# Kernel tuning notes

Measured on AMD Instinct MI355X. Metric: run time of the kernel, lower is better.

Reference implementation:

```python
import jax, jax.numpy as jnp
import numpy as np

B, H, W, C = 2, 192, 192, 192
WS, SHIFT, NH = 16, 8, 6


def _window_partition(x, ws):
    b, h, w, c = x.shape
    x = x.reshape(b, h // ws, ws, w // ws, ws, c)
    return x.transpose(0, 1, 3, 2, 4, 5).reshape(-1, ws, ws, c)


def _window_reverse(win, ws, h, w):
    b = win.shape[0] // ((h // ws) * (w // ws))
    x = win.reshape(b, h // ws, w // ws, ws, ws, -1)
    return x.transpose(0, 1, 3, 2, 4, 5).reshape(b, h, w, -1)


def _relative_position_index(ws):
    coords = np.stack(np.meshgrid(np.arange(ws), np.arange(ws), indexing="ij"))
    cf = coords.reshape(2, -1)
    rel = (cf[:, :, None] - cf[:, None, :]).transpose(1, 2, 0).astype(np.int64)
    rel[..., 0] += ws - 1
    rel[..., 1] += ws - 1
    rel[..., 0] *= 2 * ws - 1
    return rel.sum(-1)  # (ws*ws, ws*ws) in [0, (2ws-1)^2)


def _shift_attn_mask(h, w, ws, shift):
    img = np.zeros((1, h, w, 1), np.float32)
    cnt = 0
    for hs in (slice(0, -ws), slice(-ws, -shift), slice(-shift, None)):
        for wsl in (slice(0, -ws), slice(-ws, -shift), slice(-shift, None)):
            img[:, hs, wsl, :] = cnt
            cnt += 1
    mw = np.asarray(_window_partition(jnp.asarray(img), ws)).reshape(-1, ws * ws)
    diff = mw[:, None, :] - mw[:, :, None]
    return jnp.asarray(np.where(diff != 0, -100.0, 0.0).astype(np.float32))


def setup_inputs():
    key = jax.random.key(0)
    ks = jax.random.split(key, 4)
    x = jax.random.normal(ks[0], (B, H, W, C), jnp.float32)
    qkv = jax.random.normal(ks[1], (B, H, W, 3 * C), jnp.float32)
    rpb_table = 0.02 * jax.random.normal(ks[2], ((2 * WS - 1) ** 2, NH), jnp.float32)
    geo_scale = jnp.full((NH,), 0.01, jnp.float32)
    geo_sigma = jnp.asarray(1.0, jnp.float32)
    proj_w = 0.02 * jax.random.normal(ks[3], (C, C), jnp.float32)
    proj_b = jnp.zeros((C,), jnp.float32)
    rpi = jnp.asarray(_relative_position_index(WS), jnp.int32)
    attn_mask = _shift_attn_mask(H, W, WS, SHIFT)
    return dict(x=x, qkv=qkv, rpb_table=rpb_table, geo_scale=geo_scale,
                geo_sigma=geo_sigma, proj_w=proj_w, proj_b=proj_b,
                rpi=rpi, attn_mask=attn_mask,
                window_size=WS, shift_size=SHIFT, num_heads=NH)


def _geo_bias(f, ws, sigma):
    # f: (nwb, ws, ws, C). L-shaped geodesic path: horizontal then vertical cumsums.
    nwb = f.shape[0]
    diff_h = jnp.sum(jnp.abs(f[:, :, 1:] - f[:, :, :-1]), -1)  # (nwb, ws, ws-1)
    ct_h = jnp.cumsum(jnp.concatenate(
        [jnp.zeros((nwb, ws, 1), f.dtype), 1.0 + sigma * diff_h], -1), -1)
    diff_v = jnp.sum(jnp.abs(f[:, 1:] - f[:, :-1]), -1)        # (nwb, ws-1, ws)
    ct_v = jnp.cumsum(jnp.concatenate(
        [jnp.zeros((nwb, 1, ws), f.dtype), 1.0 + sigma * diff_v], -2), -2)
    idx = jnp.arange(ws * ws)
    rows, cols = idx // ws, idx % ws
    ct_h_flat = ct_h[:, rows, cols]                    # (nwb, n)
    ct_v_flat = ct_v[:, rows, cols]
    ct_h_corner = ct_h[:, rows[:, None], cols[None, :]]  # ct_h[ri, cj] -> (nwb, n, n)
    ct_v_corner = ct_v[:, rows[:, None], cols[None, :]]
    geo_h = jnp.abs(ct_h_corner - ct_h_flat[:, :, None])
    geo_v = jnp.abs(ct_v_flat[:, None, :] - ct_v_corner)
    return geo_h + geo_v                               # (nwb, n, n)


def _forward(x, qkv, rpb_table, geo_scale, geo_sigma, proj_w, proj_b,
             rpi, attn_mask, ws, shift, nh):
    b, h, w, c = x.shape
    n = ws * ws
    hd = c // nh
    sx = jnp.roll(x, (-shift, -shift), (1, 2))
    sqkv = jnp.roll(qkv, (-shift, -shift), (1, 2))
    f_win = _window_partition(sx, ws)                           # (nwb, ws, ws, c)
    geo = _geo_bias(f_win, ws, jnp.abs(geo_sigma))              # (nwb, n, n)
    qkv_win = _window_partition(sqkv, ws).reshape(-1, n, 3, nh, hd)
    q = qkv_win[:, :, 0].transpose(0, 2, 1, 3)                  # (nwb, nh, n, hd)
    k = qkv_win[:, :, 1].transpose(0, 2, 1, 3)
    v = qkv_win[:, :, 2].transpose(0, 2, 1, 3)
    attn = jnp.einsum("bhqd,bhkd->bhqk", q * (hd ** -0.5), k)   # (nwb, nh, n, n)
    rpb = rpb_table[rpi.reshape(-1)].reshape(n, n, nh).transpose(2, 0, 1)
    attn = attn + rpb[None]
    attn = attn - geo[:, None] * geo_scale[None, :, None, None]
    nw = attn_mask.shape[0]
    attn = attn.reshape(b, nw, nh, n, n) + attn_mask[None, :, None]
    attn = jax.nn.softmax(attn.reshape(-1, nh, n, n), axis=-1)
    out = jnp.einsum("bhqk,bhkd->bqhd", attn, v).reshape(-1, n, c)
    out = out @ proj_w.T + proj_b                               # nn.Linear
    out = _window_reverse(out.reshape(-1, ws, ws, c), ws, h, w)
    out = jnp.roll(out, (shift, shift), (1, 2))
    return out.reshape(b, h * w, c)


def reference(x, qkv, rpb_table, geo_scale, geo_sigma, proj_w, proj_b,
              rpi, attn_mask, window_size, shift_size, num_heads):
    return _forward(x, qkv, rpb_table, geo_scale, geo_sigma, proj_w, proj_b,
                    rpi, attn_mask, window_size, shift_size, num_heads)
```

## Files before the change

### kernel.cpp

```cpp
#include <hip/hip_runtime.h>
#include <stdint.h>

#define HH 192
#define WWW 192
#define CC 192
#define WS 16
#define SHIFTS 8
#define NH 6
#define HD 32
#define NN 256
#define NWS 12
#define NWIN_B 144
#define NWIN 288
#define CTN (NWIN * NN)

typedef _Float16 half_t;
typedef half_t half2_t __attribute__((ext_vector_type(2)));
typedef half_t f16x8 __attribute__((ext_vector_type(8)));
typedef float f32x4 __attribute__((ext_vector_type(4)));
typedef uint32_t u32x4 __attribute__((ext_vector_type(4)));

#define LOG2E 1.4426950408889634f

#if __has_builtin(__builtin_amdgcn_exp2f)
#define EXP2F(x) __builtin_amdgcn_exp2f(x)
#else
#define EXP2F(x) __expf(0.6931471805599453f * (x))
#endif

__device__ __forceinline__ float sat16(float a) {
    return fminf(fmaxf(a, -60000.f), 60000.f);
}
__device__ __forceinline__ uint32_t pack_h2(float a, float b) {
    half2_t h; h.x = (half_t)sat16(a); h.y = (half_t)sat16(b);
    return __builtin_bit_cast(uint32_t, h);
}
__device__ __forceinline__ uint32_t pack_p(float a, float b) {
    half2_t h; h.x = (half_t)a; h.y = (half_t)b;
    return __builtin_bit_cast(uint32_t, h);
}

__device__ __forceinline__ size_t xrow(int b, int sh, int sw) {
    int oh = sh + SHIFTS; if (oh >= HH) oh -= HH;
    int ow = sw + SHIFTS; if (ow >= WWW) ow -= WWW;
    return ((size_t)((b * HH + oh) * WWW + ow)) * CC;
}
__device__ __forceinline__ size_t qkvrow(int b, int sh, int sw) {
    int oh = sh + SHIFTS; if (oh >= HH) oh -= HH;
    int ow = sw + SHIFTS; if (ow >= WWW) ow -= WWW;
    return ((size_t)((b * HH + oh) * WWW + ow)) * (3 * CC);
}
__device__ __forceinline__ int regof(int v) { return v < (HH - WS) ? 0 : (v < (HH - SHIFTS) ? 1 : 2); }

__device__ __forceinline__ float* ctptr(float* o, int q) {
    int slot = q / 96;
    int off = q - slot * 96;
    return o + (size_t)slot * CC + 96 + off;
}

__global__ __launch_bounds__(512) void kgeo(const float* __restrict__ x,
                                            const float* __restrict__ sigp,
                                            float* __restrict__ outbuf) {
    __shared__ float xs[96][256];
    __shared__ float dh[2][16][16];
    __shared__ float dv[2][16][16];
    int win = blockIdx.x;
    int b = win / NWIN_B, wi = win % NWIN_B;
    int wr = wi / NWS, wc = wi % NWS;
    int t = threadIdx.x;
    int tok = t & 255, hf = t >> 8;
    int r = tok >> 4, j = tok & 15;
    int tj1 = (j < 15) ? tok + 1 : tok;
    int tr1 = (r < 15) ? tok + 16 : tok;

    int stok = t >> 1;
    size_t srow = xrow(b, wr * WS + (stok >> 4), wc * WS + (stok & 15));

    float sh_ = 0.f, sv_ = 0.f;
    #pragma unroll
    for (int ck = 0; ck < 2; ck++) {
        __syncthreads();
        const float4* src = (const float4*)(x + srow + ck * 96) + (t & 1) * 12;
        int cbase = (t & 1) * 48;
        #pragma unroll
        for (int i = 0; i < 12; i++) {
            float4 u = src[i];
            int c = cbase + i * 4;
            xs[c + 0][stok] = u.x; xs[c + 1][stok] = u.y;
            xs[c + 2][stok] = u.z; xs[c + 3][stok] = u.w;
        }
        __syncthreads();
        int c0 = hf * 48;
        #pragma unroll 8
        for (int c = 0; c < 48; c++) {
            float a = xs[c0 + c][tok];
            sh_ += fabsf(xs[c0 + c][tj1] - a);
            sv_ += fabsf(xs[c0 + c][tr1] - a);
        }
    }
    dh[hf][r][j] = (j < 15) ? sh_ : 0.f;
    dv[hf][r][j] = (r < 15) ? sv_ : 0.f;
    __syncthreads();

    float sigma = fabsf(sigp[0]);
    if (t < 16) {
        float acc = 0.f;
        *ctptr(outbuf, win * NN + t * 16) = 0.f;
        for (int jj = 1; jj < 16; jj++) {
            acc += 1.0f + sigma * (dh[0][t][jj - 1] + dh[1][t][jj - 1]);
            *ctptr(outbuf, win * NN + t * 16 + jj) = acc;
        }
    } else if (t < 32) {
        int c = t - 16;
        float acc = 0.f;
        *ctptr(outbuf, CTN + win * NN + c) = 0.f;
        for (int ii = 1; ii < 16; ii++) {
            acc += 1.0f + sigma * (dv[0][ii - 1][c] + dv[1][ii - 1][c]);
            *ctptr(outbuf, CTN + win * NN + ii * 16 + c) = acc;
        }
    }
}

__global__ __launch_bounds__(512, 4) void kattn(const float* __restrict__ qkv,
                                                const float* __restrict__ rpb_table,
                                                const float* __restrict__ geo_scale,
                                                float* __restrict__ outbuf) {
    __shared__ __align__(16) uint32_t Klds[256 * 20];
    __shared__ __align__(16) uint32_t Vt[32 * 140];
    __shared__ __align__(16) float cth_s[NN];
    __shared__ __align__(16) float ctv_s[NN];
    __shared__ float rpb_s[961];

    int win = blockIdx.x, head = blockIdx.y;
    int b = win / NWIN_B, wi = win % NWIN_B;
    int wr = wi / NWS, wc = wi % NWS;
    int wr16 = wr * WS, wc16 = wc * WS;
    int t = threadIdx.x;
    int dl = t & 15;
    int g = (t >> 4) & 3;
    int g4 = g * 4;
    int w = t >> 6;

    for (int i = t; i < 961; i += 512) rpb_s[i] = rpb_table[i * NH + head] * LOG2E;

    if (t < 256) {
        int r = t >> 4, c = t & 15;
        const float4* k4 = (const float4*)(qkv + qkvrow(b, wr16 + r, wc16 + c) + CC + head * HD);
        uint32_t kp[16];
        #pragma unroll
        for (int c4 = 0; c4 < 8; c4++) {
            float4 u = k4[c4];
            kp[c4 * 2 + 0] = pack_h2(u.x, u.y);
            kp[c4 * 2 + 1] = pack_h2(u.z, u.w);
        }
        uint4* dst = (uint4*)((char*)Klds + t * 80);
        #pragma unroll
        for (int i = 0; i < 4; i++)
            dst[i] = make_uint4(kp[i * 4 + 0], kp[i * 4 + 1], kp[i * 4 + 2], kp[i * 4 + 3]);
    } else if (t < 384) {
        int tv = t - 256;
        int p0 = 2 * tv, p1 = 2 * tv + 1;
        const float4* v0 = (const float4*)(qkv + qkvrow(b, wr16 + (p0 >> 4), wc16 + (p0 & 15)) + 2 * CC + head * HD);
        const float4* v1 = (const float4*)(qkv + qkvrow(b, wr16 + (p1 >> 4), wc16 + (p1 & 15)) + 2 * CC + head * HD);
        #pragma unroll
        for (int c4 = 0; c4 < 8; c4++) {
            float4 a = v0[c4], bu = v1[c4];
            Vt[(c4 * 4 + 0) * 140 + tv] = pack_h2(a.x, bu.x);
            Vt[(c4 * 4 + 1) * 140 + tv] = pack_h2(a.y, bu.y);
            Vt[(c4 * 4 + 2) * 140 + tv] = pack_h2(a.z, bu.z);
            Vt[(c4 * 4 + 3) * 140 + tv] = pack_h2(a.w, bu.w);
        }
    } else {
        int tc = t - 384;
        cth_s[tc]       = *ctptr(outbuf, win * NN + tc);
        cth_s[tc + 128] = *ctptr(outbuf, win * NN + tc + 128);
        ctv_s[tc]       = *ctptr(outbuf, CTN + win * NN + tc);
        ctv_s[tc + 128] = *ctptr(outbuf, CTN + win * NN + tc + 128);
    }
    f16x8 qf[2];
    #pragma unroll
    for (int qt = 0; qt < 2; qt++) {
        const float* qp = qkv + qkvrow(b, wr16 + 2 * w + qt, wc16 + dl) + head * HD + g * 8;
        float4 u0 = ((const float4*)qp)[0];
        float4 u1 = ((const float4*)qp)[1];
        f16x8 q8;
        q8[0] = (half_t)sat16(u0.x); q8[1] = (half_t)sat16(u0.y);
        q8[2] = (half_t)sat16(u0.z); q8[3] = (half_t)sat16(u0.w);
        q8[4] = (half_t)sat16(u1.x); q8[5] = (half_t)sat16(u1.y);
        q8[6] = (half_t)sat16(u1.z); q8[7] = (half_t)sat16(u1.w);
        qf[qt] = q8;
    }
    __syncthreads();

    float gscale2 = geo_scale[head] * LOG2E;
    float ghs[2][4];
    f32x4 Dv[2];
    int regq[2], qb0[2];
    #pragma unroll
    for (int qt = 0; qt < 2; qt++) {
        int rq = 2 * w + qt;
        float chq = cth_s[rq * 16 + dl];
        f32x4 Bv = *(const f32x4*)&cth_s[rq * 16 + g4];
        Dv[qt] = *(const f32x4*)&ctv_s[rq * 16 + g4];
        #pragma unroll
        for (int r = 0; r < 4; r++) ghs[qt][r] = -gscale2 * fabsf(Bv[r] - chq);
        regq[qt] = 3 * regof(wr16 + rq) + regof(wc16 + dl);
        qb0[qt] = rq * 31 + dl + 480 - g4;
    }
    int regkc[4];
    #pragma unroll
    for (int r = 0; r < 4; r++) regkc[r] = regof(wc16 + g4 + r);
    const float scale2 = 0.17677669529663687f * LOG2E;

    f32x4 o[2][2];
    #pragma unroll
    for (int qt = 0; qt < 2; qt++) { o[qt][0] = (f32x4){0.f,0.f,0.f,0.f}; o[qt][1] = (f32x4){0.f,0.f,0.f,0.f}; }
    float lq[2] = {0.f, 0.f};

    const char* KB = (const char*)Klds;
    const char* VB = (const char*)Vt;
    const f32x4 zf = {0.f, 0.f, 0.f, 0.f};
    int srcA = ((g & 1) << 5) + dl;
    int srcB = srcA + 16;
    bool hi = (g >= 2);

#define KVLOOP(MASKED)                                                                  \
    _Pragma("unroll 2")                                                                 \
    for (int kvb = 0; kvb < 8; kvb++) {                                                 \
        int kv0 = kvb * 32;                                                             \
        f16x8 ak0 = *(const f16x8*)(KB + (size_t)(kv0 + dl) * 80 + g * 16);             \
        f16x8 ak1 = *(const f16x8*)(KB + (size_t)(kv0 + 16 + dl) * 80 + g * 16);        \
        f32x4 s[2][2];                                                                  \
        s[0][0] = __builtin_amdgcn_mfma_f32_16x16x32_f16(ak0, qf[0], zf, 0, 0, 0);      \
        s[0][1] = __builtin_amdgcn_mfma_f32_16x16x32_f16(ak1, qf[0], zf, 0, 0, 0);      \
        s[1][0] = __builtin_amdgcn_mfma_f32_16x16x32_f16(ak0, qf[1], zf, 0, 0, 0);      \
        s[1][1] = __builtin_amdgcn_mfma_f32_16x16x32_f16(ak1, qf[1], zf, 0, 0, 0);      \
        f32x4 cv0 = *(const f32x4*)&ctv_s[kv0 + g4];                                    \
        f32x4 cv1 = *(const f32x4*)&ctv_s[kv0 + 16 + g4];                               \
        uint32_t pkk[2][2][2];                                                          \
        _Pragma("unroll")                                                               \
        for (int qt = 0; qt < 2; qt++) {                                                \
            _Pragma("unroll")                                                           \
            for (int kt = 0; kt < 2; kt++) {                                            \
                int rk = kvb * 2 + kt;                                                  \
                int rowreg = MASKED ? 3 * regof(wr16 + rk) : 0;                         \
                int idxk = qb0[qt] - rk * 31;                                           \
                float pr[4];                                                            \
                _Pragma("unroll")                                                       \
                for (int r = 0; r < 4; r++) {                                           \
                    float C = kt ? cv1[r] : cv0[r];                                     \
                    float geoV = fabsf(C - Dv[qt][r]);                                  \
                    float bias = rpb_s[idxk - r] + ghs[qt][r];                          \
                    if (MASKED)                                                         \
                        bias += ((rowreg + regkc[r] == regq[qt]) ? 0.f : -100.f * LOG2E); \
                    float tt2 = fmaf(s[qt][kt][r], scale2, fmaf(-gscale2, geoV, bias)); \
                    tt2 = fminf(fmaxf(tt2, -1000.f), 15.f);                             \
                    float p = EXP2F(tt2);                                               \
                    lq[qt] += p;                                                        \
                    pr[r] = p;                                                          \
                }                                                                       \
                pkk[qt][kt][0] = pack_p(pr[0], pr[1]);                                  \
                pkk[qt][kt][1] = pack_p(pr[2], pr[3]);                                  \
            }                                                                           \
        }                                                                               \
        f16x8 bv0 = *(const f16x8*)(VB + (size_t)dl * 560 + kv0 * 2 + g * 16);          \
        f16x8 bv1 = *(const f16x8*)(VB + (size_t)(16 + dl) * 560 + kv0 * 2 + g * 16);   \
        _Pragma("unroll")                                                               \
        for (int qt = 0; qt < 2; qt++) {                                                \
            uint32_t a00 = __shfl((int)pkk[qt][0][0], srcA), a01 = __shfl((int)pkk[qt][0][1], srcA); \
            uint32_t a10 = __shfl((int)pkk[qt][0][0], srcB), a11 = __shfl((int)pkk[qt][0][1], srcB); \
            uint32_t b00 = __shfl((int)pkk[qt][1][0], srcA), b01 = __shfl((int)pkk[qt][1][1], srcA); \
            uint32_t b10 = __shfl((int)pkk[qt][1][0], srcB), b11 = __shfl((int)pkk[qt][1][1], srcB); \
            u32x4 uu;                                                                   \
            uu.x = hi ? b00 : a00; uu.y = hi ? b01 : a01;                               \
            uu.z = hi ? b10 : a10; uu.w = hi ? b11 : a11;                               \
            f16x8 ap = __builtin_bit_cast(f16x8, uu);                                   \
            o[qt][0] = __builtin_amdgcn_mfma_f32_16x16x32_f16(ap, bv0, o[qt][0], 0, 0, 0); \
            o[qt][1] = __builtin_amdgcn_mfma_f32_16x16x32_f16(ap, bv1, o[qt][1], 0, 0, 0); \
        }                                                                               \
    }

    if (wr < 11 && wc < 11) {
        KVLOOP(false)
    } else {
        KVLOOP(true)
    }
#undef KVLOOP

    float invr[2][4];
    #pragma unroll
    for (int qt = 0; qt < 2; qt++) {
        float li = lq[qt];
        li += __shfl_xor(li, 16);
        li += __shfl_xor(li, 32);
        float iv = 1.0f / li;
        #pragma unroll
        for (int r = 0; r < 4; r++) invr[qt][r] = __shfl(iv, g4 + r);
    }

    __syncthreads();
    char* OB = (char*)Klds + w * 2560;
    #pragma unroll
    for (int qt = 0; qt < 2; qt++)
        #pragma unroll
        for (int dt = 0; dt < 2; dt++)
            #pragma unroll
            for (int r = 0; r < 4; r++) {
                float val = o[qt][dt][r] * invr[qt][r];
                *(half_t*)(OB + (qt * 16 + g4 + r) * 80 + (dt * 16 + dl) * 2) = (half_t)sat16(val);
            }

    int lane = t & 63;
    int lp = lane >> 1, half = lane & 1;
    int tok = 32 * w + lp;
    int rr = tok >> 4, pc = tok & 15;
    int oh = wr16 + rr + SHIFTS; if (oh >= HH) oh -= HH;
    int ow = wc16 + pc + SHIFTS; if (ow >= WWW) ow -= WWW;
    size_t R = (size_t)b * (HH * WWW) + (size_t)oh * WWW + ow;
    uint4* o4p = (uint4*)outbuf;
    const uint4* src = (const uint4*)(OB + lp * 80 + half * 32);
    size_t base4 = R * 48 + head * 4 + half * 2;
    o4p[base4 + 0] = src[0];
    o4p[base4 + 1] = src[1];
}

__global__ __launch_bounds__(512, 4) void kproj(float* __restrict__ data,
                                                const float* __restrict__ proj_w,
                                                const float* __restrict__ proj_b) {
    __shared__ __align__(16) uint32_t Wh[192 * 100];
    int t = threadIdx.x;
    size_t R0 = (size_t)blockIdx.x * 128;

    const float4* pw4 = (const float4*)proj_w;
    for (int q = t; q < 9216; q += 512) {
        int j = q / 48, c4 = q - j * 48;
        float4 u = pw4[q];
        *(uint2*)&Wh[j * 100 + c4 * 2] = make_uint2(pack_h2(u.x, u.y), pack_h2(u.z, u.w));
    }
    __syncthreads();

    int dl = t & 15, g = (t >> 4) & 3, w = t >> 6;
    const char* WB = (const char*)Wh;
    const char* AB = (const char*)data;

    f32x4 acc[12];
    #pragma unroll
    for (int i = 0; i < 12; i++) acc[i] = (f32x4){0.f, 0.f, 0.f, 0.f};

    size_t arow = (size_t)(R0 + w * 16 + dl) * 768;
    #pragma unroll
    for (int ch = 0; ch < 6; ch++) {
        f16x8 af = *(const f16x8*)(AB + arow + ch * 64 + g * 16);
        #pragma unroll
        for (int jt = 0; jt < 12; jt++) {
            f16x8 bf = *(const f16x8*)(WB + (size_t)(jt * 16 + dl) * 400 + ch * 64 + g * 16);
            acc[jt] = __builtin_amdgcn_mfma_f32_16x16x32_f16(af, bf, acc[jt], 0, 0, 0);
        }
    }

    float bvv[12];
    #pragma unroll
    for (int jt = 0; jt < 12; jt++) bvv[jt] = proj_b[jt * 16 + dl];
    size_t orow = (size_t)(R0 + w * 16 + g * 4) * 192;
    #pragma unroll
    for (int jt = 0; jt < 12; jt++)
        #pragma unroll
        for (int r = 0; r < 4; r++)
            data[orow + (size_t)r * 192 + jt * 16 + dl] = acc[jt][r] + bvv[jt];
}

extern "C" void kernel_launch(void* const* d_in, const int* in_sizes, int n_in,
                              void* d_out, int out_size, void* d_ws, size_t ws_size,
                              hipStream_t stream) {
    const float *x = nullptr, *qkv = nullptr, *rpb = nullptr, *gsc = nullptr,
                *pw = nullptr, *pb = nullptr, *sig = nullptr;
    for (int i = 0; i < n_in; i++) {
        switch (in_sizes[i]) {
            case 14155776: x   = (const float*)d_in[i]; break;
            case 42467328: qkv = (const float*)d_in[i]; break;
            case 5766:     rpb = (const float*)d_in[i]; break;
            case 6:        gsc = (const float*)d_in[i]; break;
            case 36864:    pw  = (const float*)d_in[i]; break;
            case 192:      pb  = (const float*)d_in[i]; break;
            default: break;
        }
    }
    if (n_in > 4 && in_sizes[4] == 1) sig = (const float*)d_in[4];
    else for (int i = 0; i < n_in; i++) if (in_sizes[i] == 1) { sig = (const float*)d_in[i]; break; }
    if (!x)   x   = (const float*)d_in[0];
    if (!qkv) qkv = (const float*)d_in[1];
    if (!rpb) rpb = (const float*)d_in[2];
    if (!gsc) gsc = (const float*)d_in[3];
    if (!sig) sig = (const float*)d_in[4];
    if (!pw)  pw  = (const float*)d_in[5];
    if (!pb)  pb  = (const float*)d_in[6];

    float* out = (float*)d_out;

    kgeo<<<dim3(NWIN), dim3(512), 0, stream>>>(x, sig, out);
    kattn<<<dim3(NWIN, NH), dim3(512), 0, stream>>>(qkv, rpb, gsc, out);
    kproj<<<dim3((NWIN * NN) / 128), dim3(512), 0, stream>>>(out, pw, pb);
}
```

Measured before the change: 395.8 us.

## Permute K rows so softmax P feeds PV MFMA directly, drop shuffles

Reorders which K rows feed each QK MFMA lane group so that the output register layout of the score tile already matches the A-operand layout needed by the PV MFMA. This removes the eight cross-lane shuffles per q-tile per kv block. The relative-position bias table is re-laid out as pre-reversed float4 groups, so each bias fetch becomes one vector LDS load instead of four scalar ones. The mask row term is now computed once per kv block. In exchange, more per-thread geo and bias index registers are precomputed, and the index arithmetic has to be exactly right for correctness.

Result: faster. 375.6 us (-5.1%).

```diff
diff --git a/kernel.cpp b/kernel.cpp
--- a/kernel.cpp
+++ b/kernel.cpp
@@ -129,7 +129,7 @@
     __shared__ __align__(16) uint32_t Vt[32 * 140];
     __shared__ __align__(16) float cth_s[NN];
     __shared__ __align__(16) float ctv_s[NN];
-    __shared__ float rpb_s[961];
+    __shared__ __align__(16) float rpbT[868 * 4];
 
     int win = blockIdx.x, head = blockIdx.y;
     int b = win / NWIN_B, wi = win % NWIN_B;
@@ -138,10 +138,18 @@
     int t = threadIdx.x;
     int dl = t & 15;
     int g = (t >> 4) & 3;
-    int g4 = g * 4;
     int w = t >> 6;
 
-    for (int i = t; i < 961; i += 512) rpb_s[i] = rpb_table[i * NH + head] * LOG2E;
+    for (int e = t; e < 868; e += 512) {
+        int u = e / 28, m12 = e - u * 28;
+        int base = u * 31 + m12 + 3;
+        float4 v;
+        v.x = rpb_table[(base    ) * NH + head] * LOG2E;
+        v.y = rpb_table[(base - 1) * NH + head] * LOG2E;
+        v.z = rpb_table[(base - 2) * NH + head] * LOG2E;
+        v.w = rpb_table[(base - 3) * NH + head] * LOG2E;
+        *(float4*)&rpbT[e * 4] = v;
+    }
 
     if (t < 256) {
         int r = t >> 4, c = t & 15;
@@ -192,24 +200,28 @@
     }
     __syncthreads();
 
+    int g1_8 = 8 * (g & 1);
     float gscale2 = geo_scale[head] * LOG2E;
-    float ghs[2][4];
-    f32x4 Dv[2];
-    int regq[2], qb0[2];
+    f32x4 ghs[2][2];
+    f32x4 Dv[2][2];
+    int regq[2], bidx[2][2];
     #pragma unroll
     for (int qt = 0; qt < 2; qt++) {
         int rq = 2 * w + qt;
         float chq = cth_s[rq * 16 + dl];
-        f32x4 Bv = *(const f32x4*)&cth_s[rq * 16 + g4];
-        Dv[qt] = *(const f32x4*)&ctv_s[rq * 16 + g4];
-        #pragma unroll
-        for (int r = 0; r < 4; r++) ghs[qt][r] = -gscale2 * fabsf(Bv[r] - chq);
+        #pragma unroll
+        for (int kt = 0; kt < 2; kt++) {
+            f32x4 Bv = *(const f32x4*)&cth_s[rq * 16 + g1_8 + 4 * kt];
+            Dv[qt][kt] = *(const f32x4*)&ctv_s[rq * 16 + g1_8 + 4 * kt];
+            f32x4 gh;
+            #pragma unroll
+            for (int r = 0; r < 4; r++) gh[r] = -gscale2 * fabsf(Bv[r] - chq);
+            ghs[qt][kt] = gh;
+            bidx[qt][kt] = (2 * w + qt - (g >> 1) + 15) * 28 + (dl - g1_8 + 12 - 4 * kt);
+        }
         regq[qt] = 3 * regof(wr16 + rq) + regof(wc16 + dl);
-        qb0[qt] = rq * 31 + dl + 480 - g4;
-    }
-    int regkc[4];
-    #pragma unroll
-    for (int r = 0; r < 4; r++) regkc[r] = regof(wc16 + g4 + r);
+    }
+    int wk8 = wc16 + g1_8;
     const float scale2 = 0.17677669529663687f * LOG2E;
 
     f32x4 o[2][2];
@@ -220,39 +232,36 @@
     const char* KB = (const char*)Klds;
     const char* VB = (const char*)Vt;
     const f32x4 zf = {0.f, 0.f, 0.f, 0.f};
-    int srcA = ((g & 1) << 5) + dl;
-    int srcB = srcA + 16;
-    bool hi = (g >= 2);
+    int tA = 8 * (dl >> 2) + (dl & 3);
 
 #define KVLOOP(MASKED)                                                                  \
     _Pragma("unroll 2")                                                                 \
     for (int kvb = 0; kvb < 8; kvb++) {                                                 \
         int kv0 = kvb * 32;                                                             \
-        f16x8 ak0 = *(const f16x8*)(KB + (size_t)(kv0 + dl) * 80 + g * 16);             \
-        f16x8 ak1 = *(const f16x8*)(KB + (size_t)(kv0 + 16 + dl) * 80 + g * 16);        \
+        f16x8 ak0 = *(const f16x8*)(KB + (size_t)(kv0 + tA) * 80 + g * 16);             \
+        f16x8 ak1 = *(const f16x8*)(KB + (size_t)(kv0 + tA + 4) * 80 + g * 16);         \
         f32x4 s[2][2];                                                                  \
         s[0][0] = __builtin_amdgcn_mfma_f32_16x16x32_f16(ak0, qf[0], zf, 0, 0, 0);      \
         s[0][1] = __builtin_amdgcn_mfma_f32_16x16x32_f16(ak1, qf[0], zf, 0, 0, 0);      \
         s[1][0] = __builtin_amdgcn_mfma_f32_16x16x32_f16(ak0, qf[1], zf, 0, 0, 0);      \
         s[1][1] = __builtin_amdgcn_mfma_f32_16x16x32_f16(ak1, qf[1], zf, 0, 0, 0);      \
-        f32x4 cv0 = *(const f32x4*)&ctv_s[kv0 + g4];                                    \
-        f32x4 cv1 = *(const f32x4*)&ctv_s[kv0 + 16 + g4];                               \
+        f32x4 cv0 = *(const f32x4*)&ctv_s[kv0 + 8 * g];                                 \
+        f32x4 cv1 = *(const f32x4*)&ctv_s[kv0 + 8 * g + 4];                             \
+        int rowreg = MASKED ? 3 * regof(wr16 + 2 * kvb + (g >> 1)) : 0;                 \
         uint32_t pkk[2][2][2];                                                          \
         _Pragma("unroll")                                                               \
         for (int qt = 0; qt < 2; qt++) {                                                \
             _Pragma("unroll")                                                           \
             for (int kt = 0; kt < 2; kt++) {                                            \
-                int rk = kvb * 2 + kt;                                                  \
-                int rowreg = MASKED ? 3 * regof(wr16 + rk) : 0;                         \
-                int idxk = qb0[qt] - rk * 31;                                           \
+                f32x4 rv = *(const f32x4*)&rpbT[(bidx[qt][kt] - 56 * kvb) * 4];         \
                 float pr[4];                                                            \
                 _Pragma("unroll")                                                       \
                 for (int r = 0; r < 4; r++) {                                           \
                     float C = kt ? cv1[r] : cv0[r];                                     \
-                    float geoV = fabsf(C - Dv[qt][r]);                                  \
-                    float bias = rpb_s[idxk - r] + ghs[qt][r];                          \
+                    float geoV = fabsf(C - Dv[qt][kt][r]);                              \
+                    float bias = rv[r] + ghs[qt][kt][r];                                \
                     if (MASKED)                                                         \
-                        bias += ((rowreg + regkc[r] == regq[qt]) ? 0.f : -100.f * LOG2E); \
+                        bias += ((rowreg + regof(wk8 + 4 * kt + r) == regq[qt]) ? 0.f : -100.f * LOG2E); \
                     float tt2 = fmaf(s[qt][kt][r], scale2, fmaf(-gscale2, geoV, bias)); \
                     tt2 = fminf(fmaxf(tt2, -1000.f), 15.f);                             \
                     float p = EXP2F(tt2);                                               \
@@ -267,13 +276,9 @@
         f16x8 bv1 = *(const f16x8*)(VB + (size_t)(16 + dl) * 560 + kv0 * 2 + g * 16);   \
         _Pragma("unroll")                                                               \
         for (int qt = 0; qt < 2; qt++) {                                                \
-            uint32_t a00 = __shfl((int)pkk[qt][0][0], srcA), a01 = __shfl((int)pkk[qt][0][1], srcA); \
-            uint32_t a10 = __shfl((int)pkk[qt][0][0], srcB), a11 = __shfl((int)pkk[qt][0][1], srcB); \
-            uint32_t b00 = __shfl((int)pkk[qt][1][0], srcA), b01 = __shfl((int)pkk[qt][1][1], srcA); \
-            uint32_t b10 = __shfl((int)pkk[qt][1][0], srcB), b11 = __shfl((int)pkk[qt][1][1], srcB); \
             u32x4 uu;                                                                   \
-            uu.x = hi ? b00 : a00; uu.y = hi ? b01 : a01;                               \
-            uu.z = hi ? b10 : a10; uu.w = hi ? b11 : a11;                               \
+            uu.x = pkk[qt][0][0]; uu.y = pkk[qt][0][1];                                 \
+            uu.z = pkk[qt][1][0]; uu.w = pkk[qt][1][1];                                 \
             f16x8 ap = __builtin_bit_cast(f16x8, uu);                                   \
             o[qt][0] = __builtin_amdgcn_mfma_f32_16x16x32_f16(ap, bv0, o[qt][0], 0, 0, 0); \
             o[qt][1] = __builtin_amdgcn_mfma_f32_16x16x32_f16(ap, bv1, o[qt][1], 0, 0, 0); \
@@ -295,7 +300,7 @@
         li += __shfl_xor(li, 32);
         float iv = 1.0f / li;
         #pragma unroll
-        for (int r = 0; r < 4; r++) invr[qt][r] = __shfl(iv, g4 + r);
+        for (int r = 0; r < 4; r++) invr[qt][r] = __shfl(iv, g * 4 + r);
     }
 
     __syncthreads();
@@ -307,7 +312,7 @@
             #pragma unroll
             for (int r = 0; r < 4; r++) {
                 float val = o[qt][dt][r] * invr[qt][r];
-                *(half_t*)(OB + (qt * 16 + g4 + r) * 80 + (dt * 16 + dl) * 2) = (half_t)sat16(val);
+                *(half_t*)(OB + (qt * 16 + g * 4 + r) * 80 + (dt * 16 + dl) * 2) = (half_t)sat16(val);
             }
 
     int lane = t & 63;
```
